# Kernel optimization log

Hardware: AMD Instinct MI355X
Metric: run time of the kernel (lower is better)

## Reference

```python
import jax, jax.numpy as jnp
import numpy as np

N_NODES = 50000
N_GRAPHS = 64


def gcn_conv(x, W, b, src, dst, n_nodes):
    # PyG GCNConv: add self-loops, symmetric normalization D^-1/2 A D^-1/2,
    # linear transform, scatter-sum aggregation from src -> dst, plus bias.
    si = jnp.arange(n_nodes, dtype=src.dtype)
    s = jnp.concatenate([src, si])
    d = jnp.concatenate([dst, si])
    deg = jax.ops.segment_sum(jnp.ones_like(d, dtype=x.dtype), d, num_segments=n_nodes)
    dinv = jax.lax.rsqrt(jnp.maximum(deg, 1.0))  # deg >= 1 due to self-loops
    norm = dinv[s] * dinv[d]                      # [E+N]
    h = x @ W                                     # [N, out]
    msg = h[s] * norm[:, None]                    # gather + scale
    out = jax.ops.segment_sum(msg, d, num_segments=n_nodes)
    return out + b


def setup_inputs() -> dict:
    key = jax.random.key(0)
    ks = jax.random.split(key, 12)
    input_dim, hidden, half = 128, 64, 32
    x = jax.random.normal(ks[0], (N_NODES, input_dim), dtype=jnp.float32)
    edge_index = jax.random.randint(ks[1], (2, 800000), 0, N_NODES, dtype=jnp.int64)
    batch = jnp.sort(jax.random.randint(ks[2], (N_NODES,), 0, N_GRAPHS, dtype=jnp.int64))
    def lin(k, fan_in, fan_out):
        s = 1.0 / np.sqrt(fan_in)
        return jax.random.uniform(k, (fan_in, fan_out), jnp.float32, -s, s)
    return {
        "x": x,
        "edge_index": edge_index,
        "batch": batch,
        "W1": lin(ks[3], input_dim, hidden), "b1": jnp.zeros((hidden,), jnp.float32),
        "W2": lin(ks[4], hidden, hidden),    "b2": jnp.zeros((hidden,), jnp.float32),
        "Wc1": lin(ks[5], hidden, half),     "bc1": jnp.zeros((half,), jnp.float32),
        "Wc2": lin(ks[6], half, 1),          "bc2": jnp.zeros((1,), jnp.float32),
    }


def reference(x, edge_index, batch, W1, b1, W2, b2, Wc1, bc1, Wc2, bc2):
    src, dst = edge_index[0], edge_index[1]
    h = jax.nn.relu(gcn_conv(x, W1, b1, src, dst, N_NODES))
    # F.dropout(training=False) -> identity in eval
    h = jax.nn.relu(gcn_conv(h, W2, b2, src, dst, N_NODES))
    # global_mean_pool over graphs
    sums = jax.ops.segment_sum(h, batch, num_segments=N_GRAPHS)
    cnts = jax.ops.segment_sum(jnp.ones((h.shape[0], 1), h.dtype), batch, num_segments=N_GRAPHS)
    g = sums / jnp.maximum(cnts, 1.0)             # [G, hidden]
    # MLP head (Dropout(0.2) is identity in eval)
    z = jax.nn.relu(g @ Wc1 + bc1)
    return z @ Wc2 + bc2                          # [G, 1]
```

## Files before the change

### kernel.cpp

```cpp
#include <hip/hip_runtime.h>
#include <math.h>

#define NG 64
#define HID 64
#define ELL 64
#define NSCAN 16

typedef __attribute__((ext_vector_type(8))) short bf16x8;
typedef __attribute__((ext_vector_type(4))) float f32x4;

__device__ __forceinline__ unsigned int bfbits(float f) {
    unsigned int u = __float_as_uint(f);
    return (u + 0x7FFFu + ((u >> 16) & 1u)) >> 16;
}
__device__ __forceinline__ float bfval(unsigned int bits) {
    return __uint_as_float(bits << 16);
}
__device__ __forceinline__ float dinv_of(int d) {
    return 1.0f / sqrtf((float)d + 1.0f);
}

__global__ __launch_bounds__(256) void k_prep(int* __restrict__ deg, int n,
                                              const int* __restrict__ batch,
                                              int* __restrict__ gstart,
                                              const float* __restrict__ W1,
                                              const float* __restrict__ W2,
                                              unsigned short* __restrict__ W1hi,
                                              unsigned short* __restrict__ W1lo,
                                              unsigned short* __restrict__ W2hi,
                                              unsigned short* __restrict__ W2lo) {
    int i = blockIdx.x * 256 + threadIdx.x;
    if (i < n) {
        deg[i] = 0;
        int bi = batch[i];
        int bp = (i == 0) ? -1 : batch[i - 1];
        for (int g = bp + 1; g <= bi; ++g) gstart[g] = i;
        if (i == n - 1)
            for (int g = bi + 1; g <= NG; ++g) gstart[g] = n;
    }
    if (i < 128 * 64) {
        int k = i >> 6, c = i & 63;
        float f = W1[i];
        unsigned hb = bfbits(f);
        W1hi[c * 128 + k] = (unsigned short)hb;
        W1lo[c * 128 + k] = (unsigned short)bfbits(f - bfval(hb));
    }
    int i2 = i - 128 * 64;
    if (i2 >= 0 && i2 < 64 * 64) {
        int k = i2 >> 6, c = i2 & 63;
        float f = W2[i2];
        unsigned hb = bfbits(f);
        W2hi[c * 64 + k] = (unsigned short)hb;
        W2lo[c * 64 + k] = (unsigned short)bfbits(f - bfval(hb));
    }
}

__global__ __launch_bounds__(256) void k_degfill(const int* __restrict__ src,
                                                 const int* __restrict__ dst, int E,
                                                 int step, int n,
                                                 int* __restrict__ deg,
                                                 int* __restrict__ col_ell, int bpg) {
    const int group = blockIdx.x / bpg;
    const int blk   = blockIdx.x % bpg;
    const int lo = group * step;
    const int hi = min(lo + step, n);
    const int base = blk * 1024;
#pragma unroll
    for (int k = 0; k < 4; ++k) {
        int e = base + k * 256 + threadIdx.x;
        if (e < E) {
            int d = dst[e];
            if (d >= lo && d < hi) {
                int slot = atomicAdd(deg + d, 1);
                if (slot < ELL) col_ell[(size_t)d * ELL + slot] = src[e];
            }
        }
    }
}

template<int K>
__global__ __launch_bounds__(256) void k_gemm_mfma(const float* __restrict__ A,
                                                   const unsigned short* __restrict__ Whi,
                                                   const unsigned short* __restrict__ Wlo,
                                                   const int* __restrict__ deg,
                                                   float* __restrict__ out, int n) {
    const int wave = threadIdx.x >> 6, lane = threadIdx.x & 63;
    const int ntile2 = (n + 31) >> 5;
    const int tile2 = blockIdx.x * 4 + wave;
    if (tile2 >= ntile2) return;
    const int lrow = lane & 15;
    const int kgrp = lane >> 4;
    const int r0 = tile2 * 32 + lrow;
    const int r1 = r0 + 16;

    f32x4 acc0[4], acc1[4];
#pragma unroll
    for (int ct = 0; ct < 4; ++ct) {
        acc0[ct] = (f32x4){0.f, 0.f, 0.f, 0.f};
        acc1[ct] = (f32x4){0.f, 0.f, 0.f, 0.f};
    }

#pragma unroll
    for (int s = 0; s < K / 32; ++s) {
        float a0[8], a1[8];
        {
            const float* p0 = A + (size_t)r0 * K + s * 32 + kgrp * 8;
            const float* p1 = A + (size_t)r1 * K + s * 32 + kgrp * 8;
            float4 u0, u1, w0, w1;
            if (r0 < n) { u0 = *(const float4*)p0; u1 = *(const float4*)(p0 + 4); }
            else { u0 = make_float4(0.f,0.f,0.f,0.f); u1 = u0; }
            if (r1 < n) { w0 = *(const float4*)p1; w1 = *(const float4*)(p1 + 4); }
            else { w0 = make_float4(0.f,0.f,0.f,0.f); w1 = w0; }
            a0[0]=u0.x; a0[1]=u0.y; a0[2]=u0.z; a0[3]=u0.w;
            a0[4]=u1.x; a0[5]=u1.y; a0[6]=u1.z; a0[7]=u1.w;
            a1[0]=w0.x; a1[1]=w0.y; a1[2]=w0.z; a1[3]=w0.w;
            a1[4]=w1.x; a1[5]=w1.y; a1[6]=w1.z; a1[7]=w1.w;
        }
        bf16x8 ahi0, alo0, ahi1, alo1;
#pragma unroll
        for (int e = 0; e < 8; ++e) {
            unsigned hb0 = bfbits(a0[e]);
            ahi0[e] = (short)hb0;
            alo0[e] = (short)bfbits(a0[e] - bfval(hb0));
            unsigned hb1 = bfbits(a1[e]);
            ahi1[e] = (short)hb1;
            alo1[e] = (short)bfbits(a1[e] - bfval(hb1));
        }
#pragma unroll
        for (int ct = 0; ct < 4; ++ct) {
            const size_t wo = (size_t)(ct * 16 + lrow) * K + s * 32 + kgrp * 8;
            bf16x8 whi = *(const bf16x8*)(Whi + wo);
            bf16x8 wlo = *(const bf16x8*)(Wlo + wo);
            acc0[ct] = __builtin_amdgcn_mfma_f32_16x16x32_bf16(ahi0, whi, acc0[ct], 0, 0, 0);
            acc0[ct] = __builtin_amdgcn_mfma_f32_16x16x32_bf16(alo0, whi, acc0[ct], 0, 0, 0);
            acc0[ct] = __builtin_amdgcn_mfma_f32_16x16x32_bf16(ahi0, wlo, acc0[ct], 0, 0, 0);
            acc1[ct] = __builtin_amdgcn_mfma_f32_16x16x32_bf16(ahi1, whi, acc1[ct], 0, 0, 0);
            acc1[ct] = __builtin_amdgcn_mfma_f32_16x16x32_bf16(alo1, whi, acc1[ct], 0, 0, 0);
            acc1[ct] = __builtin_amdgcn_mfma_f32_16x16x32_bf16(ahi1, wlo, acc1[ct], 0, 0, 0);
        }
    }

#pragma unroll
    for (int r = 0; r < 4; ++r) {
        int o0 = tile2 * 32 + kgrp * 4 + r;
        if (o0 < n) {
            float dv = dinv_of(deg[o0]);
#pragma unroll
            for (int ct = 0; ct < 4; ++ct)
                out[(size_t)o0 * HID + ct * 16 + lrow] = acc0[ct][r] * dv;
        }
        int o1 = o0 + 16;
        if (o1 < n) {
            float dv = dinv_of(deg[o1]);
#pragma unroll
            for (int ct = 0; ct < 4; ++ct)
                out[(size_t)o1 * HID + ct * 16 + lrow] = acc1[ct][r] * dv;
        }
    }
}

__global__ __launch_bounds__(512) void k_gather_gemm2(const float* __restrict__ hs,
                                                      const int* __restrict__ deg,
                                                      const int* __restrict__ col_ell,
                                                      const float* __restrict__ bias,
                                                      const unsigned short* __restrict__ Whi,
                                                      const unsigned short* __restrict__ Wlo,
                                                      float* __restrict__ outB, int n) {
    __shared__ float Ash[32][68];
    const int wave = threadIdx.x >> 6, lane = threadIdx.x & 63;
    const int grp = lane >> 4, sub = lane & 15;
    const int row = wave * 4 + grp;
    const int node = blockIdx.x * 32 + row;
    const bool has = node < n;

    float4 acc = make_float4(0.f, 0.f, 0.f, 0.f);
    float di = 0.f;
    int j = 0, e = 0;
    const int* cbase = col_ell + (size_t)node * ELL;
    if (has) {
        int dg = deg[node];
        e = min(dg, ELL);
        di = dinv_of(dg);
        acc = *(const float4*)(hs + (size_t)node * HID + sub * 4);
    }
    while (__any(j < e)) {
        int cc[8];
#pragma unroll
        for (int t = 0; t < 8; ++t) cc[t] = (j + t < e) ? cbase[j + t] : -1;
        float4 vv[8];
#pragma unroll
        for (int t = 0; t < 8; ++t)
            if (cc[t] >= 0) vv[t] = *(const float4*)(hs + (size_t)cc[t] * HID + sub * 4);
#pragma unroll
        for (int t = 0; t < 8; ++t)
            if (cc[t] >= 0) {
                acc.x += vv[t].x; acc.y += vv[t].y;
                acc.z += vv[t].z; acc.w += vv[t].w;
            }
        j += 8;
    }
    {
        float4 bv = *(const float4*)(bias + sub * 4);
        float4 o;
        o.x = has ? fmaxf(fmaf(acc.x, di, bv.x), 0.f) : 0.f;
        o.y = has ? fmaxf(fmaf(acc.y, di, bv.y), 0.f) : 0.f;
        o.z = has ? fmaxf(fmaf(acc.z, di, bv.z), 0.f) : 0.f;
        o.w = has ? fmaxf(fmaf(acc.w, di, bv.w), 0.f) : 0.f;
        *(float4*)&Ash[row][sub * 4] = o;
    }
    __syncthreads();

    const int rt = wave >> 2, ct = wave & 3;
    const int lrow = lane & 15;
    const int kgrp = lane >> 4;
    f32x4 a = (f32x4){0.f, 0.f, 0.f, 0.f};
#pragma unroll
    for (int s = 0; s < 2; ++s) {
        const float* ap = &Ash[rt * 16 + lrow][s * 32 + kgrp * 8];
        float4 u0 = *(const float4*)ap;
        float4 u1 = *(const float4*)(ap + 4);
        float av[8] = {u0.x, u0.y, u0.z, u0.w, u1.x, u1.y, u1.z, u1.w};
        bf16x8 ahi, alo;
#pragma unroll
        for (int e2 = 0; e2 < 8; ++e2) {
            unsigned hb = bfbits(av[e2]);
            ahi[e2] = (short)hb;
            alo[e2] = (short)bfbits(av[e2] - bfval(hb));
        }
        const size_t wo = (size_t)(ct * 16 + lrow) * 64 + s * 32 + kgrp * 8;
        bf16x8 whi = *(const bf16x8*)(Whi + wo);
        bf16x8 wlo = *(const bf16x8*)(Wlo + wo);
        a = __builtin_amdgcn_mfma_f32_16x16x32_bf16(ahi, whi, a, 0, 0, 0);
        a = __builtin_amdgcn_mfma_f32_16x16x32_bf16(alo, whi, a, 0, 0, 0);
        a = __builtin_amdgcn_mfma_f32_16x16x32_bf16(ahi, wlo, a, 0, 0, 0);
    }
#pragma unroll
    for (int r = 0; r < 4; ++r) {
        int orow = blockIdx.x * 32 + rt * 16 + kgrp * 4 + r;
        if (orow < n)
            outB[(size_t)orow * HID + ct * 16 + lrow] = a[r] * dinv_of(deg[orow]);
    }
}

__global__ __launch_bounds__(256) void k_gather(const float* __restrict__ hs,
                                                const int* __restrict__ deg,
                                                const int* __restrict__ col_ell,
                                                const float* __restrict__ bias,
                                                float* __restrict__ out, int n) {
    const int wave = threadIdx.x >> 6, lane = threadIdx.x & 63;
    const int grp = lane >> 4, sub = lane & 15;
    const int node = blockIdx.x * 16 + wave * 4 + grp;
    const bool has = node < n;

    float4 acc = make_float4(0.f, 0.f, 0.f, 0.f);
    float di = 0.f;
    int j = 0, e = 0;
    const int* cbase = col_ell + (size_t)node * ELL;
    if (has) {
        int dg = deg[node];
        e = min(dg, ELL);
        di = dinv_of(dg);
        acc = *(const float4*)(hs + (size_t)node * HID + sub * 4);
    }
    while (__any(j < e)) {
        int cc[8];
#pragma unroll
        for (int t = 0; t < 8; ++t) cc[t] = (j + t < e) ? cbase[j + t] : -1;
        float4 vv[8];
#pragma unroll
        for (int t = 0; t < 8; ++t)
            if (cc[t] >= 0) vv[t] = *(const float4*)(hs + (size_t)cc[t] * HID + sub * 4);
#pragma unroll
        for (int t = 0; t < 8; ++t)
            if (cc[t] >= 0) {
                acc.x += vv[t].x; acc.y += vv[t].y;
                acc.z += vv[t].z; acc.w += vv[t].w;
            }
        j += 8;
    }
    if (has) {
        float4 bv = *(const float4*)(bias + sub * 4);
        float4 o;
        o.x = fmaxf(fmaf(acc.x, di, bv.x), 0.f);
        o.y = fmaxf(fmaf(acc.y, di, bv.y), 0.f);
        o.z = fmaxf(fmaf(acc.z, di, bv.z), 0.f);
        o.w = fmaxf(fmaf(acc.w, di, bv.w), 0.f);
        *(float4*)(out + (size_t)node * HID + sub * 4) = o;
    }
}

__global__ __launch_bounds__(512) void k_poolhead(const float* __restrict__ h,
                                                  const int* __restrict__ gstart,
                                                  const float* __restrict__ Wc1,
                                                  const float* __restrict__ bc1,
                                                  const float* __restrict__ Wc2,
                                                  const float* __restrict__ bc2,
                                                  float* __restrict__ outp, int n) {
    const int g = blockIdx.x;
    const int lo = gstart[g], lo2 = gstart[g + 1];
    const int t = threadIdx.x;
    const int rg = t >> 4;
    const int c4 = (t & 15) * 4;
    float4 acc = make_float4(0.f, 0.f, 0.f, 0.f);
    for (int r = lo + rg; r < lo2; r += 32) {
        float4 v = *(const float4*)(h + (size_t)r * HID + c4);
        acc.x += v.x; acc.y += v.y; acc.z += v.z; acc.w += v.w;
    }
    __shared__ float4 red[32][16];
    __shared__ float gmv[HID];
    __shared__ float zs[32];
    red[rg][t & 15] = acc;
    __syncthreads();
    if (t < 16) {
        float4 s = red[0][t];
#pragma unroll
        for (int g2 = 1; g2 < 32; ++g2) {
            float4 v = red[g2][t];
            s.x += v.x; s.y += v.y; s.z += v.z; s.w += v.w;
        }
        float inv = 1.0f / fmaxf((float)(lo2 - lo), 1.0f);
        gmv[t * 4 + 0] = s.x * inv; gmv[t * 4 + 1] = s.y * inv;
        gmv[t * 4 + 2] = s.z * inv; gmv[t * 4 + 3] = s.w * inv;
    }
    __syncthreads();
    if (t < 32) {
        float z = bc1[t];
#pragma unroll 8
        for (int k = 0; k < HID; ++k) z = fmaf(gmv[k], Wc1[k * 32 + t], z);
        zs[t] = fmaxf(z, 0.f) * Wc2[t];
    }
    __syncthreads();
    if (t == 0) {
        float o = bc2[0];
#pragma unroll
        for (int j = 0; j < 32; ++j) o += zs[j];
        outp[g] = o;
    }
}

extern "C" void kernel_launch(void* const* d_in, const int* in_sizes, int n_in,
                              void* d_out, int out_size, void* d_ws, size_t ws_size,
                              hipStream_t stream) {
    const float* x    = (const float*)d_in[0];
    const int*   ei   = (const int*)d_in[1];
    const int*   batch= (const int*)d_in[2];
    const float* W1   = (const float*)d_in[3];
    const float* b1   = (const float*)d_in[4];
    const float* W2   = (const float*)d_in[5];
    const float* b2   = (const float*)d_in[6];
    const float* Wc1  = (const float*)d_in[7];
    const float* bc1  = (const float*)d_in[8];
    const float* Wc2  = (const float*)d_in[9];
    const float* bc2  = (const float*)d_in[10];

    const int E = in_sizes[1] / 2;
    const int n = in_sizes[0] / 128;
    const int* srcp = ei;
    const int* dstp = ei + E;

    char* ws = (char*)d_ws;
    auto alloc = [&](size_t bytes) {
        char* p = ws;
        ws += (bytes + 255) & ~(size_t)255;
        return p;
    };
    int*   deg      = (int*)  alloc((size_t)n * 4);
    int*   gstart   = (int*)  alloc((size_t)(NG + 1) * 4);
    int*   col_ell  = (int*)  alloc((size_t)n * ELL * 4);
    float* bufA     = (float*)alloc((size_t)n * HID * 4);
    float* bufB     = (float*)alloc((size_t)n * HID * 4);
    unsigned short* W1hi = (unsigned short*)alloc(128 * 64 * 2);
    unsigned short* W1lo = (unsigned short*)alloc(128 * 64 * 2);
    unsigned short* W2hi = (unsigned short*)alloc(64 * 64 * 2);
    unsigned short* W2lo = (unsigned short*)alloc(64 * 64 * 2);

    const int nblk = (n + 255) / 256;
    k_prep<<<nblk, 256, 0, stream>>>(deg, n, batch, gstart,
                                     W1, W2, W1hi, W1lo, W2hi, W2lo);

    const int bpg = (E + 1023) / 1024;
    const int step = (n + NSCAN - 1) / NSCAN;
    k_degfill<<<NSCAN * bpg, 256, 0, stream>>>(srcp, dstp, E, step, n,
                                               deg, col_ell, bpg);

    const int mblocks = ((n + 31) / 32 + 3) / 4;

    k_gemm_mfma<128><<<mblocks, 256, 0, stream>>>(x, W1hi, W1lo, deg, bufA, n);
    k_gather_gemm2<<<(n + 31) / 32, 512, 0, stream>>>(bufA, deg, col_ell, b1,
                                                      W2hi, W2lo, bufB, n);
    k_gather<<<(n + 15) / 16, 256, 0, stream>>>(bufB, deg, col_ell, b2, bufA, n);

    k_poolhead<<<NG, 512, 0, stream>>>(bufA, gstart, Wc1, bc1, Wc2, bc2, (float*)d_out, n);
}
```

Before: 153.3 us.

## Fuse mean-pool into second gather via per-block segmented atomics

The second GCN aggregation now reduces its 16 output rows per block in shared memory by graph id and atomically adds partial sums into a small per-graph accumulator. This removes the write of the full layer-2 activation buffer and its re-read by a separate pooling kernel. A tiny single-block head kernel then computes the means and the MLP. The cost is float atomics, which can contend on the same graph rows and make summation order nondeterministic, plus a serial head computation in one wave.

```diff
diff --git a/kernel.cpp b/kernel.cpp
--- a/kernel.cpp
+++ b/kernel.cpp
@@ -23,6 +23,7 @@
 __global__ __launch_bounds__(256) void k_prep(int* __restrict__ deg, int n,
                                               const int* __restrict__ batch,
                                               int* __restrict__ gstart,
+                                              float* __restrict__ gsum,
                                               const float* __restrict__ W1,
                                               const float* __restrict__ W2,
                                               unsigned short* __restrict__ W1hi,
@@ -38,6 +39,7 @@
         if (i == n - 1)
             for (int g = bi + 1; g <= NG; ++g) gstart[g] = n;
     }
+    if (i < NG * HID) gsum[i] = 0.f;
     if (i < 128 * 64) {
         int k = i >> 6, c = i & 63;
         float f = W1[i];
@@ -242,14 +244,19 @@
     }
 }
 
-__global__ __launch_bounds__(256) void k_gather(const float* __restrict__ hs,
-                                                const int* __restrict__ deg,
-                                                const int* __restrict__ col_ell,
-                                                const float* __restrict__ bias,
-                                                float* __restrict__ out, int n) {
+__global__ __launch_bounds__(256) void k_gather_pool(const float* __restrict__ hs,
+                                                     const int* __restrict__ deg,
+                                                     const int* __restrict__ col_ell,
+                                                     const float* __restrict__ bias,
+                                                     const int* __restrict__ batch,
+                                                     float* __restrict__ gsum, int n) {
+    __shared__ float rows[16][68];
+    __shared__ int gb[16];
     const int wave = threadIdx.x >> 6, lane = threadIdx.x & 63;
     const int grp = lane >> 4, sub = lane & 15;
-    const int node = blockIdx.x * 16 + wave * 4 + grp;
+    const int row = wave * 4 + grp;
+    const int base = blockIdx.x * 16;
+    const int node = base + row;
     const bool has = node < n;
 
     float4 acc = make_float4(0.f, 0.f, 0.f, 0.f);
@@ -278,64 +285,56 @@
             }
         j += 8;
     }
-    if (has) {
+    {
         float4 bv = *(const float4*)(bias + sub * 4);
         float4 o;
-        o.x = fmaxf(fmaf(acc.x, di, bv.x), 0.f);
-        o.y = fmaxf(fmaf(acc.y, di, bv.y), 0.f);
-        o.z = fmaxf(fmaf(acc.z, di, bv.z), 0.f);
-        o.w = fmaxf(fmaf(acc.w, di, bv.w), 0.f);
-        *(float4*)(out + (size_t)node * HID + sub * 4) = o;
-    }
-}
-
-__global__ __launch_bounds__(512) void k_poolhead(const float* __restrict__ h,
-                                                  const int* __restrict__ gstart,
-                                                  const float* __restrict__ Wc1,
-                                                  const float* __restrict__ bc1,
-                                                  const float* __restrict__ Wc2,
-                                                  const float* __restrict__ bc2,
-                                                  float* __restrict__ outp, int n) {
-    const int g = blockIdx.x;
-    const int lo = gstart[g], lo2 = gstart[g + 1];
-    const int t = threadIdx.x;
-    const int rg = t >> 4;
-    const int c4 = (t & 15) * 4;
-    float4 acc = make_float4(0.f, 0.f, 0.f, 0.f);
-    for (int r = lo + rg; r < lo2; r += 32) {
-        float4 v = *(const float4*)(h + (size_t)r * HID + c4);
-        acc.x += v.x; acc.y += v.y; acc.z += v.z; acc.w += v.w;
-    }
-    __shared__ float4 red[32][16];
-    __shared__ float gmv[HID];
-    __shared__ float zs[32];
-    red[rg][t & 15] = acc;
+        o.x = has ? fmaxf(fmaf(acc.x, di, bv.x), 0.f) : 0.f;
+        o.y = has ? fmaxf(fmaf(acc.y, di, bv.y), 0.f) : 0.f;
+        o.z = has ? fmaxf(fmaf(acc.z, di, bv.z), 0.f) : 0.f;
+        o.w = has ? fmaxf(fmaf(acc.w, di, bv.w), 0.f) : 0.f;
+        *(float4*)&rows[row][sub * 4] = o;
+    }
+    if (threadIdx.x < 16)
+        gb[threadIdx.x] = (base + threadIdx.x < n) ? batch[base + threadIdx.x] : -1;
     __syncthreads();
-    if (t < 16) {
-        float4 s = red[0][t];
-#pragma unroll
-        for (int g2 = 1; g2 < 32; ++g2) {
-            float4 v = red[g2][t];
-            s.x += v.x; s.y += v.y; s.z += v.z; s.w += v.w;
-        }
-        float inv = 1.0f / fmaxf((float)(lo2 - lo), 1.0f);
-        gmv[t * 4 + 0] = s.x * inv; gmv[t * 4 + 1] = s.y * inv;
-        gmv[t * 4 + 2] = s.z * inv; gmv[t * 4 + 3] = s.w * inv;
-    }
-    __syncthreads();
-    if (t < 32) {
-        float z = bc1[t];
+
+    if (threadIdx.x < 64) {
+        const int c = threadIdx.x;
+        float run = 0.f;
+        int curg = gb[0];
+#pragma unroll
+        for (int r = 0; r < 16; ++r) {
+            int g = gb[r];
+            if (g < 0) break;
+            if (g != curg) {
+                atomicAdd(&gsum[curg * HID + c], run);
+                run = 0.f;
+                curg = g;
+            }
+            run += rows[r][c];
+        }
+        if (curg >= 0) atomicAdd(&gsum[curg * HID + c], run);
+    }
+}
+
+__global__ void k_head(const float* __restrict__ gsum, const int* __restrict__ gstart,
+                       const float* __restrict__ Wc1, const float* __restrict__ bc1,
+                       const float* __restrict__ Wc2, const float* __restrict__ bc2,
+                       float* __restrict__ outp) {
+    int g = threadIdx.x;
+    if (g >= NG) return;
+    float gm[HID];
+    float inv = 1.0f / fmaxf((float)(gstart[g + 1] - gstart[g]), 1.0f);
 #pragma unroll 8
-        for (int k = 0; k < HID; ++k) z = fmaf(gmv[k], Wc1[k * 32 + t], z);
-        zs[t] = fmaxf(z, 0.f) * Wc2[t];
-    }
-    __syncthreads();
-    if (t == 0) {
-        float o = bc2[0];
-#pragma unroll
-        for (int j = 0; j < 32; ++j) o += zs[j];
-        outp[g] = o;
-    }
+    for (int k = 0; k < HID; ++k) gm[k] = gsum[g * HID + k] * inv;
+    float o = bc2[0];
+    for (int jj = 0; jj < 32; ++jj) {
+        float z = bc1[jj];
+#pragma unroll 8
+        for (int k = 0; k < HID; ++k) z = fmaf(gm[k], Wc1[k * 32 + jj], z);
+        o = fmaf(fmaxf(z, 0.f), Wc2[jj], o);
+    }
+    outp[g] = o;
 }
 
 extern "C" void kernel_launch(void* const* d_in, const int* in_sizes, int n_in,
@@ -366,6 +365,7 @@
     };
     int*   deg      = (int*)  alloc((size_t)n * 4);
     int*   gstart   = (int*)  alloc((size_t)(NG + 1) * 4);
+    float* gsum     = (float*)alloc((size_t)NG * HID * 4);
     int*   col_ell  = (int*)  alloc((size_t)n * ELL * 4);
     float* bufA     = (float*)alloc((size_t)n * HID * 4);
     float* bufB     = (float*)alloc((size_t)n * HID * 4);
@@ -375,7 +375,7 @@
     unsigned short* W2lo = (unsigned short*)alloc(64 * 64 * 2);
 
     const int nblk = (n + 255) / 256;
-    k_prep<<<nblk, 256, 0, stream>>>(deg, n, batch, gstart,
+    k_prep<<<nblk, 256, 0, stream>>>(deg, n, batch, gstart, gsum,
                                      W1, W2, W1hi, W1lo, W2hi, W2lo);
 
     const int bpg = (E + 1023) / 1024;
@@ -388,7 +388,8 @@
     k_gemm_mfma<128><<<mblocks, 256, 0, stream>>>(x, W1hi, W1lo, deg, bufA, n);
     k_gather_gemm2<<<(n + 31) / 32, 512, 0, stream>>>(bufA, deg, col_ell, b1,
                                                       W2hi, W2lo, bufB, n);
-    k_gather<<<(n + 15) / 16, 256, 0, stream>>>(bufB, deg, col_ell, b2, bufA, n);
-
-    k_poolhead<<<NG, 512, 0, stream>>>(bufA, gstart, Wc1, bc1, Wc2, bc2, (float*)d_out, n);
-}
+    k_gather_pool<<<(n + 15) / 16, 256, 0, stream>>>(bufB, deg, col_ell, b2,
+                                                     batch, gsum, n);
+
+    k_head<<<1, 64, 0, stream>>>(gsum, gstart, Wc1, bc1, Wc2, bc2, (float*)d_out);
+}
```

New measurement: 180.5 us. 17.7% more time.
